# Optimization experiments

Hardware: AMD Instinct MI355X
Metric: run time of the kernel (lower is better)

## Reference

```python
import jax, jax.numpy as jnp
import numpy as np


def setup_inputs() -> dict:
    key = jax.random.key(0)
    ks = jax.random.split(key, 9)
    B, C, H, W = 16, 512, 64, 64
    s = 1.0 / np.sqrt(C)  # fan-in style init scale for 1x1 conv weights
    x = jax.random.normal(ks[0], (B, C, H, W), dtype=jnp.float32)
    W_theta = jax.random.normal(ks[1], (C, C), dtype=jnp.float32) * s
    b_theta = jax.random.normal(ks[2], (C,), dtype=jnp.float32) * 0.01
    W_phi = jax.random.normal(ks[3], (C, C), dtype=jnp.float32) * s
    b_phi = jax.random.normal(ks[4], (C,), dtype=jnp.float32) * 0.01
    W_g = jax.random.normal(ks[5], (C, C), dtype=jnp.float32) * s
    b_g = jax.random.normal(ks[6], (C,), dtype=jnp.float32) * 0.01
    W_out = jax.random.normal(ks[7], (C, C), dtype=jnp.float32) * s
    b_out = jax.random.normal(ks[8], (C,), dtype=jnp.float32) * 0.01
    return {
        "x": x,
        "W_theta": W_theta, "b_theta": b_theta,
        "W_phi": W_phi, "b_phi": b_phi,
        "W_g": W_g, "b_g": b_g,
        "W_out": W_out, "b_out": b_out,
    }


def reference(x, W_theta, b_theta, W_phi, b_phi, W_g, b_g, W_out, b_out):
    B, C, H, W = x.shape
    n = H * W
    xf = x.reshape(B, C, n)  # [B, C, HW]

    def conv1x1(Wm, b):
        # 1x1 conv == channel-mixing GEMM: [O,C] x [B,C,N] -> [B,O,N]
        return jnp.einsum('oc,bcn->bon', Wm, xf) + b[None, :, None]

    phi = conv1x1(W_phi, b_phi)      # [B, C, HW]
    theta = conv1x1(W_theta, b_theta)  # [B, C, HW] (used transposed: 'b (h w) c')
    g = conv1x1(W_g, b_g)            # [B, C, HW]

    # phi @ theta^T over spatial dim -> [B, C, C] channel-channel attention
    scores = jnp.einsum('bcn,bdn->bcd', phi, theta) * (1.0 / C)
    attn = jax.nn.softmax(scores, axis=2)  # softmax over last (dim=2), as in torch
    Y = jnp.einsum('bcd,bdn->bcn', attn, g)  # [B, C, HW]

    A = jnp.einsum('oc,bcn->bon', W_out, Y) + b_out[None, :, None]
    return x + A.reshape(B, C, H, W)
```

## Files before the change

kernel.cpp:

```cpp
#include <hip/hip_runtime.h>
#include <hip/hip_bf16.h>
#include <stdint.h>


typedef unsigned short u16;
typedef __attribute__((ext_vector_type(8))) short frag8;
typedef __attribute__((ext_vector_type(4))) float f32x4;

__device__ __forceinline__ u16 f2bf(float f) {
  union { __hip_bfloat16 h; u16 u; } c; c.h = __float2bfloat16(f); return c.u;
}

__device__ __forceinline__ void gl_lds16(const u16* g, u16* l) {
  __builtin_amdgcn_global_load_lds(
      (const __attribute__((address_space(1))) void*)g,
      (__attribute__((address_space(3))) void*)l, 16, 0, 0);
}

#define SCHED0 __builtin_amdgcn_sched_barrier(0)
#define SBAR   __builtin_amdgcn_s_barrier()

__global__ __launch_bounds__(256) void prep_x(const float* __restrict__ X,
                                              u16* __restrict__ XT,
                                              u16* __restrict__ XB,
                                              float* __restrict__ SP) {
  const int b = blockIdx.z;
  const int n0 = blockIdx.x * 64;
  const int c0 = blockIdx.y * 64;
  __shared__ u16 t[64][72];
  const float* Xb = X + (int64_t)b * (512LL * 4096);
  const int tid = threadIdx.x;
  const int r = tid >> 3;
  const int e8 = (tid & 7) * 8;
#pragma unroll
  for (int p = 0; p < 2; p++) {
    const int row = p * 32 + r;
    const int c = c0 + row;
    const float4 f0 = *(const float4*)(Xb + (int64_t)c * 4096 + n0 + e8);
    const float4 f1 = *(const float4*)(Xb + (int64_t)c * 4096 + n0 + e8 + 4);
    union { uint4 q; u16 u[8]; } pk;
    pk.u[0] = f2bf(f0.x); pk.u[1] = f2bf(f0.y); pk.u[2] = f2bf(f0.z); pk.u[3] = f2bf(f0.w);
    pk.u[4] = f2bf(f1.x); pk.u[5] = f2bf(f1.y); pk.u[6] = f2bf(f1.z); pk.u[7] = f2bf(f1.w);
    *(uint4*)(XB + ((int64_t)b * 512 + c) * 4096 + n0 + e8) = pk.q;
    *(uint4*)&t[row][e8 ^ (row & 56)] = pk.q;
    float s = f0.x + f0.y + f0.z + f0.w + f1.x + f1.y + f1.z + f1.w;
    s += __shfl_xor(s, 1); s += __shfl_xor(s, 2); s += __shfl_xor(s, 4);
    if ((tid & 7) == 0)
      SP[((int64_t)b * 512 + c) * 64 + blockIdx.x] = s;
  }
  __syncthreads();
#pragma unroll
  for (int p = 0; p < 2; p++) {
    const int nr = p * 32 + r;
    union { uint4 q; u16 u[8]; } o;
#pragma unroll
    for (int j = 0; j < 8; j++)
      o.u[j] = t[e8 + j][nr ^ e8];
    *(uint4*)(XT + ((int64_t)b * 4096 + n0 + nr) * 512 + c0 + e8) = o.q;
  }
}

__constant__ const int g_ty[10] = {0,0,0,0,1,1,1,2,2,3};
__constant__ const int g_tx[10] = {0,1,2,3,1,2,3,2,3,3};

__global__ __launch_bounds__(256) void gram_sk(const u16* __restrict__ XB,
                                               float* __restrict__ P) {
  const int z = blockIdx.z;
  const int b = z >> 2, sp = z & 3;
  const int tl = blockIdx.x;
  const int m0 = g_ty[tl] * 128, n0 = g_tx[tl] * 128;
  const int tid = threadIdx.x;
  const int lane = tid & 63, wave = tid >> 6;
  __shared__ u16 sA[3][4096];
  __shared__ u16 sB[3][4096];
  const u16* Xb = XB + (int64_t)b * (512LL * 4096) + sp * 1024;

  f32x4 acc[4][4];
#pragma unroll
  for (int i = 0; i < 4; i++)
#pragma unroll
    for (int j = 0; j < 4; j++)
#pragma unroll
      for (int r = 0; r < 4; r++) acc[i][j][r] = 0.0f;

  const int fr = lane & 15;
  const int fkx = (((lane >> 4) ^ ((fr >> 1) & 3))) * 8;
  const int wm = (wave & 1) * 64, wn = (wave >> 1) * 64;

  const int srow = tid >> 2;
  const int scol = (((tid & 3) ^ ((tid >> 3) & 3))) * 8;
  const u16* Ar0 = Xb + (int64_t)(m0 + srow) * 4096 + scol;
  const u16* Ar1 = Xb + (int64_t)(m0 + 64 + srow) * 4096 + scol;
  const u16* Br0 = Xb + (int64_t)(n0 + srow) * 4096 + scol;
  const u16* Br1 = Xb + (int64_t)(n0 + 64 + srow) * 4096 + scol;

  auto stage = [&](int t, int buf) {
    gl_lds16(Ar0 + t * 32, sA[buf] + tid * 8);
    gl_lds16(Ar1 + t * 32, sA[buf] + 2048 + tid * 8);
    gl_lds16(Br0 + t * 32, sB[buf] + tid * 8);
    gl_lds16(Br1 + t * 32, sB[buf] + 2048 + tid * 8);
  };
  auto comp = [&](int buf) {
    frag8 af[4], bf[4];
#pragma unroll
    for (int i = 0; i < 4; i++) {
      af[i] = *(const frag8*)(sA[buf] + (wm + i * 16 + fr) * 32 + fkx);
      bf[i] = *(const frag8*)(sB[buf] + (wn + i * 16 + fr) * 32 + fkx);
    }
#pragma unroll
    for (int i = 0; i < 4; i++)
#pragma unroll
      for (int j = 0; j < 4; j++)
        acc[i][j] = __builtin_amdgcn_mfma_f32_16x16x32_bf16(af[i], bf[j], acc[i][j], 0, 0, 0);
  };

  stage(0, 0); stage(1, 1);
#pragma unroll
  for (int t = 0; t < 30; t++) {
    SCHED0; SBAR; SCHED0;
    stage(t + 2, (t + 2) % 3);
    asm volatile("s_waitcnt vmcnt(8)" ::: "memory");
    SBAR; SCHED0;
    comp(t % 3);
  }
  asm volatile("s_waitcnt vmcnt(0)" ::: "memory");
  SBAR; SCHED0;
  comp(30 % 3); comp(31 % 3);

  float* Pz = P + (int64_t)z * 262144;
  const int quad = lane >> 4;
#pragma unroll
  for (int i = 0; i < 4; i++)
#pragma unroll
    for (int j = 0; j < 4; j++) {
      const int row0 = m0 + wm + i * 16 + quad * 4;
      const int col = n0 + wn + j * 16 + fr;
#pragma unroll
      for (int r = 0; r < 4; r++)
        Pz[(int64_t)(row0 + r) * 512 + col] = acc[i][j][r];
      if (m0 != n0)
        *(f32x4*)(Pz + (int64_t)col * 512 + row0) = acc[i][j];
    }
}

__global__ __launch_bounds__(256) void reduce_G(const float* __restrict__ P,
                                                u16* __restrict__ G) {
  const int64_t t = (int64_t)blockIdx.x * 256 + threadIdx.x;
  const int b = (int)(t >> 16);
  const int64_t i = (t & 65535) * 4;
  const float* P0 = P + ((int64_t)b * 4) * 262144 + i;
  const float4 a = *(const float4*)(P0);
  const float4 c = *(const float4*)(P0 + 262144);
  const float4 d = *(const float4*)(P0 + 2 * 262144);
  const float4 e = *(const float4*)(P0 + 3 * 262144);
  union { u16 u[4]; uint2 v; } o;
  o.u[0] = f2bf(a.x + c.x + d.x + e.x);
  o.u[1] = f2bf(a.y + c.y + d.y + e.y);
  o.u[2] = f2bf(a.z + c.z + d.z + e.z);
  o.u[3] = f2bf(a.w + c.w + d.w + e.w);
  *(uint2*)(G + (int64_t)b * 262144 + i) = o.v;
}

enum { EPI_BF16 = 0, EPI_SCORES = 1, EPI_BF16I = 2 };

template <int EPI>
__global__ __launch_bounds__(256) void gemm128_bt(
    const u16* __restrict__ A, int64_t sAb, int lda,
    const u16* __restrict__ B, int64_t sBb, int ldb,
    void* __restrict__ Cv, int64_t sCb, int ldc,
    const float* __restrict__ e_bphi, const float* __restrict__ e_btheta,
    const float* __restrict__ e_uphi, const float* __restrict__ e_utheta) {
  const int b = blockIdx.z;
  const int m0 = blockIdx.y * 128, n0 = blockIdx.x * 128;
  const int tid = threadIdx.x;
  const int lane = tid & 63, wave = tid >> 6;
  __shared__ u16 sA[4][4096];
  __shared__ u16 sB[4][4096];
  const u16* Ab = A + (int64_t)b * sAb;
  const u16* Bb = B + (int64_t)b * sBb;

  f32x4 acc[4][4];
#pragma unroll
  for (int i = 0; i < 4; i++)
#pragma unroll
    for (int j = 0; j < 4; j++)
#pragma unroll
      for (int r = 0; r < 4; r++) acc[i][j][r] = 0.0f;

  const int srow = tid >> 2;
  const int scol = (((tid & 3) ^ ((tid >> 3) & 3))) * 8;
  const int fr = lane & 15;
  const int fkx = (((lane >> 4) ^ ((fr >> 1) & 3))) * 8;
  const int wm = (wave & 1) * 64, wn = (wave >> 1) * 64;

  const u16* Ar0 = Ab + (int64_t)(m0 + srow) * lda + scol;
  const u16* Ar1 = Ab + (int64_t)(m0 + 64 + srow) * lda + scol;
  const u16* Br0 = Bb + (int64_t)(n0 + srow) * ldb + scol;
  const u16* Br1 = Bb + (int64_t)(n0 + 64 + srow) * ldb + scol;

  auto stage = [&](int t, int buf) {
    gl_lds16(Ar0 + t * 32, sA[buf] + tid * 8);
    gl_lds16(Ar1 + t * 32, sA[buf] + 2048 + tid * 8);
    gl_lds16(Br0 + t * 32, sB[buf] + tid * 8);
    gl_lds16(Br1 + t * 32, sB[buf] + 2048 + tid * 8);
  };
  auto comp = [&](int buf) {
    frag8 af[4], bf[4];
#pragma unroll
    for (int i = 0; i < 4; i++) {
      af[i] = *(const frag8*)(sA[buf] + (wm + i * 16 + fr) * 32 + fkx);
      bf[i] = *(const frag8*)(sB[buf] + (wn + i * 16 + fr) * 32 + fkx);
    }
#pragma unroll
    for (int i = 0; i < 4; i++)
#pragma unroll
      for (int j = 0; j < 4; j++)
        acc[i][j] = __builtin_amdgcn_mfma_f32_16x16x32_bf16(af[i], bf[j], acc[i][j], 0, 0, 0);
  };

  stage(0, 0); stage(1, 1); stage(2, 2);
#pragma unroll
  for (int t = 0; t < 13; t++) {
    SCHED0; SBAR; SCHED0;
    stage(t + 3, (t + 3) % 4);
    asm volatile("s_waitcnt vmcnt(12)" ::: "memory");
    SBAR; SCHED0;
    comp(t % 4);
  }
  asm volatile("s_waitcnt vmcnt(8)" ::: "memory");
  SBAR; SCHED0;
  comp(13 % 4);
  asm volatile("s_waitcnt vmcnt(4)" ::: "memory");
  SBAR; SCHED0;
  comp(14 % 4);
  asm volatile("s_waitcnt vmcnt(0)" ::: "memory");
  SBAR; SCHED0;
  comp(15 % 4);

  const int quad = lane >> 4;
#pragma unroll
  for (int i = 0; i < 4; i++)
#pragma unroll
    for (int j = 0; j < 4; j++)
#pragma unroll
      for (int r = 0; r < 4; r++) {
        const int row = m0 + wm + i * 16 + quad * 4 + r;
        const int col = n0 + wn + j * 16 + fr;
        const float a = acc[i][j][r];
        if constexpr (EPI == EPI_BF16) {
          ((u16*)Cv)[(int64_t)b * sCb + (int64_t)row * ldc + col] = f2bf(a);
        } else if constexpr (EPI == EPI_BF16I) {
          ((u16*)Cv)[(int64_t)b * sCb + (int64_t)row * ldc + col] =
              f2bf(a + (row == col ? 1.0f : 0.0f));
        } else {
          const float bp = e_bphi[row];
          const float bt = e_btheta[col];
          ((float*)Cv)[(int64_t)b * sCb + (int64_t)row * ldc + col] =
              (a + bp * e_utheta[b * 512 + col] + bt * e_uphi[b * 512 + row] +
               4096.0f * bp * bt) * (1.0f / 512.0f);
        }
      }
}

__global__ __launch_bounds__(256) void gemm_final(const u16* __restrict__ M,
                                                  const u16* __restrict__ XT,
                                                  const float* __restrict__ V,
                                                  float* __restrict__ O) {
  const int b = blockIdx.z;
  const int m0 = blockIdx.y * 128, n0 = blockIdx.x * 128;
  const int tid = threadIdx.x;
  const int lane = tid & 63, wave = tid >> 6;
  __shared__ u16 sA[2][4096];
  __shared__ u16 sB[2][4096];
  const u16* Ab = M + (int64_t)b * 262144;
  const u16* Bb = XT + (int64_t)b * (4096LL * 512);

  f32x4 acc[4][4];
#pragma unroll
  for (int i = 0; i < 4; i++)
#pragma unroll
    for (int j = 0; j < 4; j++)
#pragma unroll
      for (int r = 0; r < 4; r++) acc[i][j][r] = 0.0f;

  const int srow = tid >> 2;
  const int scol = (((tid & 3) ^ ((tid >> 3) & 3))) * 8;
  const int fr = lane & 15;
  const int fkx = (((lane >> 4) ^ ((fr >> 1) & 3))) * 8;
  const int wm = (wave & 1) * 64, wn = (wave >> 1) * 64;

  const u16* Ar0 = Ab + (int64_t)(m0 + srow) * 512 + scol;
  const u16* Ar1 = Ab + (int64_t)(m0 + 64 + srow) * 512 + scol;
  const u16* Br0 = Bb + (int64_t)(n0 + srow) * 512 + scol;
  const u16* Br1 = Bb + (int64_t)(n0 + 64 + srow) * 512 + scol;

  gl_lds16(Ar0, sA[0] + tid * 8);
  gl_lds16(Ar1, sA[0] + 2048 + tid * 8);
  gl_lds16(Br0, sB[0] + tid * 8);
  gl_lds16(Br1, sB[0] + 2048 + tid * 8);
  __syncthreads();

  for (int k0 = 0; k0 < 512; k0 += 32) {
    const int cur = (k0 >> 5) & 1;
    if (k0 + 32 < 512) {
      u16* dA = sA[cur ^ 1];
      u16* dB = sB[cur ^ 1];
      gl_lds16(Ar0 + k0 + 32, dA + tid * 8);
      gl_lds16(Ar1 + k0 + 32, dA + 2048 + tid * 8);
      gl_lds16(Br0 + k0 + 32, dB + tid * 8);
      gl_lds16(Br1 + k0 + 32, dB + 2048 + tid * 8);
    }
    frag8 af[4], bf[4];
#pragma unroll
    for (int i = 0; i < 4; i++) {
      af[i] = *(const frag8*)(sA[cur] + (wm + i * 16 + fr) * 32 + fkx);
      bf[i] = *(const frag8*)(sB[cur] + (wn + i * 16 + fr) * 32 + fkx);
    }
#pragma unroll
    for (int i = 0; i < 4; i++)
#pragma unroll
      for (int j = 0; j < 4; j++)
        acc[i][j] = __builtin_amdgcn_mfma_f32_16x16x32_bf16(af[i], bf[j], acc[i][j], 0, 0, 0);
    __syncthreads();
  }

  const int quad = lane >> 4;
#pragma unroll
  for (int i = 0; i < 4; i++)
#pragma unroll
    for (int j = 0; j < 4; j++)
#pragma unroll
      for (int r = 0; r < 4; r++) {
        const int row = m0 + wm + i * 16 + quad * 4 + r;
        const int col = n0 + wn + j * 16 + fr;
        O[(int64_t)b * (512LL * 4096) + (int64_t)row * 4096 + col] =
            acc[i][j][r] + V[b * 512 + row];
      }
}

__global__ __launch_bounds__(512) void uv_kernel(const float* __restrict__ Wphi,
                                                 const float* __restrict__ Wtheta,
                                                 const float* __restrict__ SP,
                                                 float* __restrict__ UPH, float* __restrict__ UTH) {
  const int b = blockIdx.x;
  const int o = threadIdx.x;
  __shared__ float s[512];
  const float* sp = SP + ((int64_t)b * 512 + o) * 64;
  float a = 0.f;
#pragma unroll
  for (int g = 0; g < 64; g += 4) {
    const float4 q = *(const float4*)(sp + g);
    a += q.x + q.y + q.z + q.w;
  }
  s[o] = a;
  __syncthreads();
  float a0 = 0.f, a1 = 0.f;
  for (int c4 = 0; c4 < 512; c4 += 4) {
    const float4 wa = *(const float4*)(Wphi + o * 512 + c4);
    const float4 wb = *(const float4*)(Wtheta + o * 512 + c4);
    a0 += wa.x * s[c4] + wa.y * s[c4 + 1] + wa.z * s[c4 + 2] + wa.w * s[c4 + 3];
    a1 += wb.x * s[c4] + wb.y * s[c4 + 1] + wb.z * s[c4 + 2] + wb.w * s[c4 + 3];
  }
  UPH[b * 512 + o] = a0;
  UTH[b * 512 + o] = a1;
}

__global__ __launch_bounds__(512) void v_kernel(const float* __restrict__ Wout,
                                                const float* __restrict__ R,
                                                const float* __restrict__ bout,
                                                float* __restrict__ V) {
  const int b = blockIdx.x;
  const int o = threadIdx.x;
  __shared__ float s[512];
  s[o] = R[b * 512 + o];
  __syncthreads();
  float a0 = 0.f;
  for (int c4 = 0; c4 < 512; c4 += 4) {
    const float4 wa = *(const float4*)(Wout + o * 512 + c4);
    a0 += wa.x * s[c4] + wa.y * s[c4 + 1] + wa.z * s[c4 + 2] + wa.w * s[c4 + 3];
  }
  V[b * 512 + o] = a0 + bout[o];
}

__global__ __launch_bounds__(256) void convert_w(const float* __restrict__ W0,
                                                 const float* __restrict__ W1,
                                                 const float* __restrict__ W2,
                                                 u16* __restrict__ O0, u16* __restrict__ O1,
                                                 u16* __restrict__ O2) {
  const int idx = blockIdx.x * 256 + threadIdx.x;
  const int m = idx >> 16;
  const int off = (idx & 65535) * 4;
  const float* src = (m == 0) ? W0 : (m == 1) ? W1 : W2;
  u16* dst = (m == 0) ? O0 : (m == 1) ? O1 : O2;
  const float4 f = *(const float4*)(src + off);
  union { u16 u[4]; uint2 v; } p;
  p.u[0] = f2bf(f.x); p.u[1] = f2bf(f.y); p.u[2] = f2bf(f.z); p.u[3] = f2bf(f.w);
  *(uint2*)(dst + off) = p.v;
}

__global__ void wg_transpose(const float* __restrict__ Wg, u16* __restrict__ WgT) {
  __shared__ float t[16][17];
  const int i0 = blockIdx.y * 16, j0 = blockIdx.x * 16;
  t[threadIdx.y][threadIdx.x] = Wg[(i0 + threadIdx.y) * 512 + j0 + threadIdx.x];
  __syncthreads();
  WgT[(j0 + threadIdx.y) * 512 + i0 + threadIdx.x] = f2bf(t[threadIdx.x][threadIdx.y]);
}

__global__ __launch_bounds__(64) void softmax_k(float* __restrict__ SC,
                                                const float* __restrict__ bg,
                                                float* __restrict__ R) {
  const int row = blockIdx.x;
  const int lane = threadIdx.x;
  float* Sr = SC + (int64_t)row * 512;
  union { float4 q[2]; float v[8]; } u;
  u.q[0] = *(const float4*)(Sr + lane * 8);
  u.q[1] = *(const float4*)(Sr + lane * 8 + 4);
  const float4 g0 = *(const float4*)(bg + lane * 8);
  const float4 g1 = *(const float4*)(bg + lane * 8 + 4);
  const float gb[8] = { g0.x, g0.y, g0.z, g0.w, g1.x, g1.y, g1.z, g1.w };
  float m = u.v[0];
#pragma unroll
  for (int j = 1; j < 8; j++) m = fmaxf(m, u.v[j]);
#pragma unroll
  for (int off = 32; off > 0; off >>= 1) m = fmaxf(m, __shfl_xor(m, off));
  float e[8], s = 0.f, sb = 0.f;
#pragma unroll
  for (int j = 0; j < 8; j++) {
    e[j] = __expf(u.v[j] - m);
    s += e[j];
    sb += e[j] * gb[j];
  }
#pragma unroll
  for (int off = 32; off > 0; off >>= 1) { s += __shfl_xor(s, off); sb += __shfl_xor(sb, off); }
  const float inv = 1.0f / s;
  union { uint4 q; u16 h[8]; } o;
#pragma unroll
  for (int j = 0; j < 8; j++) o.h[j] = f2bf(e[j] * inv);
  *(uint4*)((u16*)SC + (int64_t)row * 1024 + lane * 8) = o.q;
  if (lane == 0) R[row] = sb * inv;
}

extern "C" void kernel_launch(void* const* d_in, const int* in_sizes, int n_in,
                              void* d_out, int out_size, void* d_ws, size_t ws_size,
                              hipStream_t stream) {
  const float* x      = (const float*)d_in[0];
  const float* Wtheta = (const float*)d_in[1];
  const float* btheta = (const float*)d_in[2];
  const float* Wphi   = (const float*)d_in[3];
  const float* bphi   = (const float*)d_in[4];
  const float* Wg     = (const float*)d_in[5];
  const float* bg     = (const float*)d_in[6];
  const float* Wout   = (const float*)d_in[7];
  const float* bout   = (const float*)d_in[8];

  char* ws = (char*)d_ws;
  u16*   xT     = (u16*)(ws + 0);
  u16*   G      = (u16*)(ws + 67108864);
  u16*   T1     = (u16*)(ws + 75497472);
  float* SC     = (float*)(ws + 83886080);
  u16*   Wphib  = (u16*)(ws + 100663296);
  u16*   Wthetab= (u16*)(ws + 101187584);
  u16*   Woutb  = (u16*)(ws + 101711872);
  u16*   WgTb   = (u16*)(ws + 102236160);
  float* UPH    = (float*)(ws + 102793216);
  float* UTH    = (float*)(ws + 102825984);
  float* R      = (float*)(ws + 102858752);
  float* V      = (float*)(ws + 102891520);
  u16* ATT = (u16*)SC;
  u16* Q = G;
  u16* M = T1;

  u16*   XB = (u16*)d_out;
  float* P  = (float*)((char*)d_out + 67108864);
  float* SP = P;

  prep_x<<<dim3(64, 8, 16), 256, 0, stream>>>(x, xT, XB, SP);
  uv_kernel<<<16, 512, 0, stream>>>(Wphi, Wtheta, SP, UPH, UTH);
  convert_w<<<768, 256, 0, stream>>>(Wphi, Wtheta, Wout, Wphib, Wthetab, Woutb);
  wg_transpose<<<dim3(32, 32), dim3(16, 16), 0, stream>>>(Wg, WgTb);
  gram_sk<<<dim3(10, 1, 64), 256, 0, stream>>>(XB, P);
  reduce_G<<<4096, 256, 0, stream>>>(P, G);
  gemm128_bt<EPI_BF16><<<dim3(4, 4, 16), 256, 0, stream>>>(
      Wphib, 0, 512, G, 512LL * 512, 512, T1, 512LL * 512, 512,
      nullptr, nullptr, nullptr, nullptr);
  gemm128_bt<EPI_SCORES><<<dim3(4, 4, 16), 256, 0, stream>>>(
      T1, 512LL * 512, 512, Wthetab, 0, 512, SC, 512LL * 512, 512,
      bphi, btheta, UPH, UTH);
  softmax_k<<<8192, 64, 0, stream>>>(SC, bg, R);
  gemm128_bt<EPI_BF16><<<dim3(4, 4, 16), 256, 0, stream>>>(
      WgTb, 0, 512, ATT, 512LL * 1024, 1024, Q, 512LL * 512, 512,
      nullptr, nullptr, nullptr, nullptr);
  gemm128_bt<EPI_BF16I><<<dim3(4, 4, 16), 256, 0, stream>>>(
      Woutb, 0, 512, Q, 512LL * 512, 512, M, 512LL * 512, 512,
      nullptr, nullptr, nullptr, nullptr);
  v_kernel<<<16, 512, 0, stream>>>(Wout, R, bout, V);
  gemm_final<<<dim3(32, 4, 16), 256, 0, stream>>>(M, xT, V, (float*)d_out);
}
```

Measured before the change: 544.8 us.

## Drop split-K in gram kernel, atomically reduce row sums, parallelize GEMV kernels

The Gram kernel no longer splits the spatial reduction four ways into fp32 partials followed by a separate reduce kernel. Each block now runs the full 4096-long K loop and writes bf16 output directly, which removes the partial-buffer traffic and one launch but leaves only 160 blocks, far fewer than before. Row sums in prep_x are accumulated with atomicAdd into a zeroed buffer instead of being written as per-tile partials. The uv and v GEMV kernels are spread over 8 times more blocks, with 4 threads per output row combined by shuffles.

New measurement: 453.6 us. 1.2x faster.

```diff
diff --git a/kernel.cpp b/kernel.cpp
--- a/kernel.cpp
+++ b/kernel.cpp
@@ -23,7 +23,7 @@
 __global__ __launch_bounds__(256) void prep_x(const float* __restrict__ X,
                                               u16* __restrict__ XT,
                                               u16* __restrict__ XB,
-                                              float* __restrict__ SP) {
+                                              float* __restrict__ S) {
   const int b = blockIdx.z;
   const int n0 = blockIdx.x * 64;
   const int c0 = blockIdx.y * 64;
@@ -45,8 +45,7 @@
     *(uint4*)&t[row][e8 ^ (row & 56)] = pk.q;
     float s = f0.x + f0.y + f0.z + f0.w + f1.x + f1.y + f1.z + f1.w;
     s += __shfl_xor(s, 1); s += __shfl_xor(s, 2); s += __shfl_xor(s, 4);
-    if ((tid & 7) == 0)
-      SP[((int64_t)b * 512 + c) * 64 + blockIdx.x] = s;
+    if ((tid & 7) == 0) atomicAdd(&S[b * 512 + c], s);
   }
   __syncthreads();
 #pragma unroll
@@ -64,16 +63,15 @@
 __constant__ const int g_tx[10] = {0,1,2,3,1,2,3,2,3,3};
 
 __global__ __launch_bounds__(256) void gram_sk(const u16* __restrict__ XB,
-                                               float* __restrict__ P) {
-  const int z = blockIdx.z;
-  const int b = z >> 2, sp = z & 3;
+                                               u16* __restrict__ G) {
+  const int b = blockIdx.z;
   const int tl = blockIdx.x;
   const int m0 = g_ty[tl] * 128, n0 = g_tx[tl] * 128;
   const int tid = threadIdx.x;
   const int lane = tid & 63, wave = tid >> 6;
   __shared__ u16 sA[3][4096];
   __shared__ u16 sB[3][4096];
-  const u16* Xb = XB + (int64_t)b * (512LL * 4096) + sp * 1024;
+  const u16* Xb = XB + (int64_t)b * (512LL * 4096);
 
   f32x4 acc[4][4];
 #pragma unroll
@@ -115,8 +113,7 @@
   };
 
   stage(0, 0); stage(1, 1);
-#pragma unroll
-  for (int t = 0; t < 30; t++) {
+  for (int t = 0; t < 126; t++) {
     SCHED0; SBAR; SCHED0;
     stage(t + 2, (t + 2) % 3);
     asm volatile("s_waitcnt vmcnt(8)" ::: "memory");
@@ -125,9 +122,10 @@
   }
   asm volatile("s_waitcnt vmcnt(0)" ::: "memory");
   SBAR; SCHED0;
-  comp(30 % 3); comp(31 % 3);
-
-  float* Pz = P + (int64_t)z * 262144;
+  comp(0);
+  comp(1);
+
+  u16* Gb = G + (int64_t)b * 262144;
   const int quad = lane >> 4;
 #pragma unroll
   for (int i = 0; i < 4; i++)
@@ -135,30 +133,16 @@
     for (int j = 0; j < 4; j++) {
       const int row0 = m0 + wm + i * 16 + quad * 4;
       const int col = n0 + wn + j * 16 + fr;
-#pragma unroll
-      for (int r = 0; r < 4; r++)
-        Pz[(int64_t)(row0 + r) * 512 + col] = acc[i][j][r];
+      union { u16 u[4]; uint2 v; } mg;
+#pragma unroll
+      for (int r = 0; r < 4; r++) {
+        const u16 h = f2bf(acc[i][j][r]);
+        Gb[(int64_t)(row0 + r) * 512 + col] = h;
+        mg.u[r] = h;
+      }
       if (m0 != n0)
-        *(f32x4*)(Pz + (int64_t)col * 512 + row0) = acc[i][j];
+        *(uint2*)(Gb + (int64_t)col * 512 + row0) = mg.v;
     }
-}
-
-__global__ __launch_bounds__(256) void reduce_G(const float* __restrict__ P,
-                                                u16* __restrict__ G) {
-  const int64_t t = (int64_t)blockIdx.x * 256 + threadIdx.x;
-  const int b = (int)(t >> 16);
-  const int64_t i = (t & 65535) * 4;
-  const float* P0 = P + ((int64_t)b * 4) * 262144 + i;
-  const float4 a = *(const float4*)(P0);
-  const float4 c = *(const float4*)(P0 + 262144);
-  const float4 d = *(const float4*)(P0 + 2 * 262144);
-  const float4 e = *(const float4*)(P0 + 3 * 262144);
-  union { u16 u[4]; uint2 v; } o;
-  o.u[0] = f2bf(a.x + c.x + d.x + e.x);
-  o.u[1] = f2bf(a.y + c.y + d.y + e.y);
-  o.u[2] = f2bf(a.z + c.z + d.z + e.z);
-  o.u[3] = f2bf(a.w + c.w + d.w + e.w);
-  *(uint2*)(G + (int64_t)b * 262144 + i) = o.v;
 }
 
 enum { EPI_BF16 = 0, EPI_SCORES = 1, EPI_BF16I = 2 };
@@ -338,48 +322,54 @@
       }
 }
 
-__global__ __launch_bounds__(512) void uv_kernel(const float* __restrict__ Wphi,
+__global__ __launch_bounds__(256) void uv_kernel(const float* __restrict__ Wphi,
                                                  const float* __restrict__ Wtheta,
-                                                 const float* __restrict__ SP,
+                                                 const float* __restrict__ S,
                                                  float* __restrict__ UPH, float* __restrict__ UTH) {
   const int b = blockIdx.x;
-  const int o = threadIdx.x;
+  const int o0 = blockIdx.y * 64;
+  const int tid = threadIdx.x;
   __shared__ float s[512];
-  const float* sp = SP + ((int64_t)b * 512 + o) * 64;
-  float a = 0.f;
-#pragma unroll
-  for (int g = 0; g < 64; g += 4) {
-    const float4 q = *(const float4*)(sp + g);
-    a += q.x + q.y + q.z + q.w;
-  }
-  s[o] = a;
+  s[tid] = S[b * 512 + tid];
+  s[tid + 256] = S[b * 512 + tid + 256];
   __syncthreads();
+  const int o = o0 + (tid >> 2);
+  const int q = tid & 3;
   float a0 = 0.f, a1 = 0.f;
-  for (int c4 = 0; c4 < 512; c4 += 4) {
-    const float4 wa = *(const float4*)(Wphi + o * 512 + c4);
-    const float4 wb = *(const float4*)(Wtheta + o * 512 + c4);
-    a0 += wa.x * s[c4] + wa.y * s[c4 + 1] + wa.z * s[c4 + 2] + wa.w * s[c4 + 3];
-    a1 += wb.x * s[c4] + wb.y * s[c4 + 1] + wb.z * s[c4 + 2] + wb.w * s[c4 + 3];
-  }
-  UPH[b * 512 + o] = a0;
-  UTH[b * 512 + o] = a1;
-}
-
-__global__ __launch_bounds__(512) void v_kernel(const float* __restrict__ Wout,
+  for (int c = q * 128; c < q * 128 + 128; c += 4) {
+    const float4 wa = *(const float4*)(Wphi + (int64_t)o * 512 + c);
+    const float4 wb = *(const float4*)(Wtheta + (int64_t)o * 512 + c);
+    a0 += wa.x * s[c] + wa.y * s[c + 1] + wa.z * s[c + 2] + wa.w * s[c + 3];
+    a1 += wb.x * s[c] + wb.y * s[c + 1] + wb.z * s[c + 2] + wb.w * s[c + 3];
+  }
+  a0 += __shfl_xor(a0, 1); a0 += __shfl_xor(a0, 2);
+  a1 += __shfl_xor(a1, 1); a1 += __shfl_xor(a1, 2);
+  if (q == 0) {
+    UPH[b * 512 + o] = a0;
+    UTH[b * 512 + o] = a1;
+  }
+}
+
+__global__ __launch_bounds__(256) void v_kernel(const float* __restrict__ Wout,
                                                 const float* __restrict__ R,
                                                 const float* __restrict__ bout,
                                                 float* __restrict__ V) {
   const int b = blockIdx.x;
-  const int o = threadIdx.x;
+  const int o0 = blockIdx.y * 64;
+  const int tid = threadIdx.x;
   __shared__ float s[512];
-  s[o] = R[b * 512 + o];
+  s[tid] = R[b * 512 + tid];
+  s[tid + 256] = R[b * 512 + tid + 256];
   __syncthreads();
+  const int o = o0 + (tid >> 2);
+  const int q = tid & 3;
   float a0 = 0.f;
-  for (int c4 = 0; c4 < 512; c4 += 4) {
-    const float4 wa = *(const float4*)(Wout + o * 512 + c4);
-    a0 += wa.x * s[c4] + wa.y * s[c4 + 1] + wa.z * s[c4 + 2] + wa.w * s[c4 + 3];
-  }
-  V[b * 512 + o] = a0 + bout[o];
+  for (int c = q * 128; c < q * 128 + 128; c += 4) {
+    const float4 wa = *(const float4*)(Wout + (int64_t)o * 512 + c);
+    a0 += wa.x * s[c] + wa.y * s[c + 1] + wa.z * s[c + 2] + wa.w * s[c + 3];
+  }
+  a0 += __shfl_xor(a0, 1); a0 += __shfl_xor(a0, 2);
+  if (q == 0) V[b * 512 + o] = a0 + bout[o];
 }
 
 __global__ __launch_bounds__(256) void convert_w(const float* __restrict__ W0,
@@ -462,6 +452,7 @@
   u16*   Wthetab= (u16*)(ws + 101187584);
   u16*   Woutb  = (u16*)(ws + 101711872);
   u16*   WgTb   = (u16*)(ws + 102236160);
+  float* S      = (float*)(ws + 102760448);
   float* UPH    = (float*)(ws + 102793216);
   float* UTH    = (float*)(ws + 102825984);
   float* R      = (float*)(ws + 102858752);
@@ -471,15 +462,13 @@
   u16* M = T1;
 
   u16*   XB = (u16*)d_out;
-  float* P  = (float*)((char*)d_out + 67108864);
-  float* SP = P;
-
-  prep_x<<<dim3(64, 8, 16), 256, 0, stream>>>(x, xT, XB, SP);
-  uv_kernel<<<16, 512, 0, stream>>>(Wphi, Wtheta, SP, UPH, UTH);
+
+  hipMemsetAsync(S, 0, 32768, stream);
+  prep_x<<<dim3(64, 8, 16), 256, 0, stream>>>(x, xT, XB, S);
+  uv_kernel<<<dim3(16, 8), 256, 0, stream>>>(Wphi, Wtheta, S, UPH, UTH);
   convert_w<<<768, 256, 0, stream>>>(Wphi, Wtheta, Wout, Wphib, Wthetab, Woutb);
   wg_transpose<<<dim3(32, 32), dim3(16, 16), 0, stream>>>(Wg, WgTb);
-  gram_sk<<<dim3(10, 1, 64), 256, 0, stream>>>(XB, P);
-  reduce_G<<<4096, 256, 0, stream>>>(P, G);
+  gram_sk<<<dim3(10, 1, 16), 256, 0, stream>>>(XB, G);
   gemm128_bt<EPI_BF16><<<dim3(4, 4, 16), 256, 0, stream>>>(
       Wphib, 0, 512, G, 512LL * 512, 512, T1, 512LL * 512, 512,
       nullptr, nullptr, nullptr, nullptr);
@@ -493,6 +482,6 @@
   gemm128_bt<EPI_BF16I><<<dim3(4, 4, 16), 256, 0, stream>>>(
       Woutb, 0, 512, Q, 512LL * 512, 512, M, 512LL * 512, 512,
       nullptr, nullptr, nullptr, nullptr);
-  v_kernel<<<16, 512, 0, stream>>>(Wout, R, bout, V);
+  v_kernel<<<dim3(16, 8), 256, 0, stream>>>(Wout, R, bout, V);
   gemm_final<<<dim3(32, 4, 16), 256, 0, stream>>>(M, xT, V, (float*)d_out);
 }
```
